# Kernel optimization log

Measured on AMD Instinct MI355X. Metric: run time of the kernel, lower is better.

## Reference

```python
import jax, jax.numpy as jnp
import numpy as np

EMB = 384
HID = 256
HEADS = 4
HD = HID // HEADS  # 64
LAYERS = 2
M_DOCS = 32
TOTAL = 4096  # 1 query + 32 docs + 4063 sentences
LN_EPS = 1e-5


def _layernorm(x, scale, bias):
    mu = jnp.mean(x, axis=-1, keepdims=True)
    var = jnp.mean(jnp.square(x - mu), axis=-1, keepdims=True)
    return (x - mu) * jax.lax.rsqrt(var + LN_EPS) * scale + bias


def setup_inputs() -> dict:
    key = jax.random.key(0)
    ks = jax.random.split(key, 12)
    g = 0.05  # small init scale (stand-in for xavier)
    return {
        "node_embeddings": jax.random.normal(ks[0], (TOTAL, EMB), jnp.float32),
        "adj": jax.random.randint(ks[1], (TOTAL, TOTAL), 0, 2, jnp.int32),
        "num_docs": M_DOCS,
        "proj_w": jax.random.normal(ks[2], (HID, EMB), jnp.float32) * g,
        "proj_b": jnp.zeros((HID,), jnp.float32),
        "ln_scale": jnp.ones((LAYERS, HID), jnp.float32),
        "ln_bias": jnp.zeros((LAYERS, HID), jnp.float32),
        "gat_W": jax.random.normal(ks[3], (LAYERS, HEADS, HD, HID), jnp.float32) * g,
        "gat_a": jax.random.normal(ks[4], (LAYERS, HEADS, 2 * HD), jnp.float32) * g,
        "fusion_w": jax.random.normal(ks[5], (HID, 2 * HID + 2), jnp.float32) * g,
        "fusion_b": jnp.zeros((HID,), jnp.float32),
        "out_w": jax.random.normal(ks[6], (HID,), jnp.float32) * g,
        "out_b": jnp.float32(0.5),
    }


def reference(node_embeddings, adj, num_docs, proj_w, proj_b, ln_scale, ln_bias,
              gat_W, gat_a, fusion_w, fusion_b, out_w, out_b):
    T = node_embeddings.shape[0]
    M = num_docs
    N = T - 1 - M  # number of sentences
    # input projection + relu (dropout = identity in eval)
    h = jax.nn.relu(node_embeddings @ proj_w.T + proj_b)  # (T, HID)
    # query-guided sentence re-weighting
    q = h[0:1]                     # (1, HID)
    s = h[1 + M:]                  # (N, HID)
    qn = q / (jnp.linalg.norm(q, axis=1, keepdims=True) + 1e-8)
    sn = s / (jnp.linalg.norm(s, axis=1, keepdims=True) + 1e-8)
    cos = (qn @ sn.T).reshape(-1, 1)          # (N,1)
    s = s + 0.8 * q * cos
    h = jnp.concatenate([h[:1 + M], s], axis=0)
    mask = (adj == 0)[None]                   # (1,T,T)
    for i in range(LAYERS):
        res = h
        x = _layernorm(h, ln_scale[i], ln_bias[i])
        Wh = jnp.einsum('nd,hkd->hnk', x, gat_W[i])                # (H,T,HD)
        # concat-attention a.[Wh_i ; Wh_j] == a_src.Wh_i + a_dst.Wh_j
        src = jnp.einsum('hnk,hk->hn', Wh, gat_a[i, :, :HD])       # (H,T)
        dst = jnp.einsum('hnk,hk->hn', Wh, gat_a[i, :, HD:])       # (H,T)
        e = jax.nn.leaky_relu(src[:, :, None] + dst[:, None, :], 0.2)  # (H,T,T)
        e = jnp.where(mask, -jnp.inf, e)
        attn = jax.nn.softmax(e, axis=-1)                          # softmax over j
        hn = jnp.einsum('hij,hjk->hik', attn, Wh)                  # (H,T,HD)
        hcat = jnp.transpose(hn, (1, 0, 2)).reshape(T, HEADS * HD)
        h = 0.5 * jax.nn.relu(hcat) + 0.5 * res
    qh = h[0:1]
    sh = h[1 + M:]
    scores = (qh @ sh.T) / (HID ** 0.5)       # (1,N)
    aw = jax.nn.softmax(scores, axis=-1)
    awT = aw.T                                # (N,1)
    qw = qh * (awT + 0.5)                     # (N,HID)
    qnf = qh / (jnp.linalg.norm(qh, axis=1, keepdims=True) + 1e-8)
    snf = sh / (jnp.linalg.norm(sh, axis=1, keepdims=True) + 1e-8)
    cosf = (qnf @ snf.T).reshape(-1, 1)       # (N,1)
    feat = jnp.concatenate([sh, qw, cosf, awT], axis=1)  # (N, 2*HID+2)
    g = jax.nn.relu(feat @ fusion_w.T + fusion_b)
    out = g @ out_w + out_b                   # (N,)
    return out + 0.5 * cosf[:, 0]
```

## Files before the change

### kernel.cpp

```cpp
#include <hip/hip_runtime.h>
#include <hip/hip_bf16.h>
#include <stdint.h>

#define TOTAL 4096
#define EMB 384
#define MD 32
#define NDOCS (TOTAL - 1 - MD)
#define LN_EPS 1e-5f
#define NEGF (-1e30f)

typedef __hip_bfloat16 bf16;
typedef unsigned short ushort_t;
typedef __attribute__((ext_vector_type(8))) short short8;
typedef __attribute__((ext_vector_type(4))) float f32x4;
typedef __attribute__((ext_vector_type(2))) float f32x2;

__device__ __forceinline__ float ldf(const void* p, int i, int isbf) {
    return isbf ? __bfloat162float(((const bf16*)p)[i]) : ((const float*)p)[i];
}

__device__ __forceinline__ unsigned f2bf(float x) {
    return (__float_as_uint(x) + 0x8000u) >> 16;
}

__device__ __forceinline__ unsigned fenc(float f) {
    unsigned u = __float_as_uint(f);
    return (u >> 31) ? ~u : (u | 0x80000000u);
}
__device__ __forceinline__ float fdec(unsigned k) {
    return __uint_as_float((k & 0x80000000u) ? (k & 0x7FFFFFFFu) : ~k);
}

#define NTRANS ((EMB * 256 + 2 * 65536 + 514 * 256) / 256)
__global__ void k_adjmask(const int* adj, unsigned long long* maskb,
                          const uint16_t* embp, int* flag, unsigned* dmaxu,
                          const void* proj_w, const void* gat_W, const void* fusion_w,
                          float* projT, float* gatT, float* fwT) {
    __shared__ int red[4];
    int i = blockIdx.x, t = threadIdx.x;
    int w = t >> 6, l = t & 63;
    for (int c = w; c < 64; c += 4) {
        int a = adj[(size_t)i * TOTAL + c * 64 + l];
        unsigned long long m = __ballot(a != 0);
        if (l == 0) maskb[i * 64 + c] = m;
    }
    if (i == 0) {
        for (int idx = t; idx < 2048; idx += 256) dmaxu[idx] = 0x007FFFFFu;
    }
    if (i < NTRANS) {
        int cnt = 0;
        for (int k = t; k < 4096; k += 256) {
            uint16_t wd = embp[2 * k];
            int e = (wd >> 7) & 0xFF;
            if (e >= 100 && e <= 140) cnt++;
        }
        for (int o = 32; o > 0; o >>= 1) cnt += __shfl_down(cnt, o);
        if ((t & 63) == 0) red[t >> 6] = cnt;
        __syncthreads();
        int isbf = (red[0] + red[1] + red[2] + red[3] > 2048) ? 1 : 0;
        if (i == 0 && t == 0) flag[0] = isbf;
        int idx = i * 256 + t;
        if (idx < EMB * 256) {
            int d = idx >> 8, c = idx & 255;
            projT[(d >> 2) * 1024 + c * 4 + (d & 3)] = ldf(proj_w, c * EMB + d, isbf);
        } else if (idx < EMB * 256 + 2 * 65536) {
            int r = idx - EMB * 256;
            int ll = r >> 16, rem = r & 65535;
            int d = rem >> 8, c = rem & 255;
            gatT[ll * 65536 + (d >> 2) * 1024 + c * 4 + (d & 3)] =
                ldf(gat_W, ll * 65536 + c * 256 + d, isbf);
        } else {
            int r = idx - (EMB * 256 + 2 * 65536);
            int j = r >> 8, c = r & 255;
            fwT[(j >> 2) * 1024 + c * 4 + (j & 3)] = ldf(fusion_w, c * 514 + j, isbf);
        }
    }
}

#define LR 8
__global__ __launch_bounds__(512) void k_lnwh(
        const void* emb, const void* proj_b, const float* projT,
        float* h, const float* gatT, const void* ln_scale, const void* ln_bias,
        const void* gat_a, ushort_t* whswz, float* srcb, unsigned* d12g,
        unsigned* dmaxu, int layer, const int* flagp) {
    __shared__ float embs[9][EMB];
    __shared__ float xs[8][256];
    __shared__ float red[2][LR][4];
    __shared__ float qred[4];
    int isbf = flagp[0];
    int t5 = threadIdx.x;
    int t = t5 & 255, half = t5 >> 8;
    int l = t5 & 63;
    int wh = (t5 >> 6) & 3;
    int i0 = blockIdx.x * LR;
    float hv[4];
    if (layer == 0) {
        for (int idx = t5; idx < 9 * EMB; idx += 512) {
            int r = idx / EMB, d = idx % EMB;
            embs[r][d] = ldf(emb, ((r < 8) ? (i0 + r) : 0) * EMB + d, isbf);
        }
        __syncthreads();
        float bias0 = ldf(proj_b, t, isbf);
        const float4* pT4 = (const float4*)projT;
        float acc[4] = {0.f, 0.f, 0.f, 0.f};
        float qacc = 0.f;
        float4 wc = pT4[t];
        for (int k4 = 0; k4 < 96; k4++) {
            float4 wn = pT4[(k4 < 95 ? k4 + 1 : 95) * 256 + t];
            int d0 = k4 * 4;
            float4 xq = *(const float4*)&embs[8][d0];
            qacc = fmaf(xq.x, wc.x, qacc); qacc = fmaf(xq.y, wc.y, qacc);
            qacc = fmaf(xq.z, wc.z, qacc); qacc = fmaf(xq.w, wc.w, qacc);
#pragma unroll
            for (int r = 0; r < 4; r++) {
                float4 x = *(const float4*)&embs[half * 4 + r][d0];
                acc[r] = fmaf(x.x, wc.x, acc[r]); acc[r] = fmaf(x.y, wc.y, acc[r]);
                acc[r] = fmaf(x.z, wc.z, acc[r]); acc[r] = fmaf(x.w, wc.w, acc[r]);
            }
            wc = wn;
        }
        float qv = fmaxf(qacc + bias0, 0.f);
#pragma unroll
        for (int r = 0; r < 4; r++) hv[r] = fmaxf(acc[r] + bias0, 0.f);
        {
            float a = qv * qv;
            for (int o = 32; o > 0; o >>= 1) a += __shfl_down(a, o);
            if (half == 0 && l == 0) qred[wh] = a;
        }
#pragma unroll
        for (int r = 0; r < 4; r++) {
            float b = hv[r] * hv[r], c = qv * hv[r];
            for (int o = 32; o > 0; o >>= 1) { b += __shfl_down(b, o); c += __shfl_down(c, o); }
            if (l == 0) { red[0][half * 4 + r][wh] = b; red[1][half * 4 + r][wh] = c; }
        }
        __syncthreads();
        if (i0 + LR > 1 + MD) {
            float qn = sqrtf(qred[0] + qred[1] + qred[2] + qred[3]) + 1e-8f;
#pragma unroll
            for (int r = 0; r < 4; r++) {
                int rr = half * 4 + r;
                int i = i0 + rr;
                if (i >= 1 + MD) {
                    float bs = red[0][rr][0] + red[0][rr][1] + red[0][rr][2] + red[0][rr][3];
                    float cs = red[1][rr][0] + red[1][rr][1] + red[1][rr][2] + red[1][rr][3];
                    float k = 0.8f * (cs / (qn * (sqrtf(bs) + 1e-8f)));
                    hv[r] += k * qv;
                }
            }
        }
#pragma unroll
        for (int r = 0; r < 4; r++)
            h[(size_t)(i0 + half * 4 + r) * 256 + t] = hv[r];
        __syncthreads();
    } else {
#pragma unroll
        for (int r = 0; r < 4; r++)
            hv[r] = h[(size_t)(i0 + half * 4 + r) * 256 + t];
    }
    float scale = ldf(ln_scale, layer * 256 + t, isbf);
    float lbias = ldf(ln_bias, layer * 256 + t, isbf);
#pragma unroll
    for (int r = 0; r < 4; r++) {
        float a = hv[r], b = hv[r] * hv[r];
        for (int o = 32; o > 0; o >>= 1) { a += __shfl_down(a, o); b += __shfl_down(b, o); }
        if (l == 0) { red[0][half * 4 + r][wh] = a; red[1][half * 4 + r][wh] = b; }
    }
    __syncthreads();
#pragma unroll
    for (int r = 0; r < 4; r++) {
        int rr = half * 4 + r;
        float mu = (red[0][rr][0] + red[0][rr][1] + red[0][rr][2] + red[0][rr][3]) * (1.f / 256.f);
        float var = (red[1][rr][0] + red[1][rr][1] + red[1][rr][2] + red[1][rr][3]) * (1.f / 256.f) - mu * mu;
        xs[rr][t] = (hv[r] - mu) * rsqrtf(var + LN_EPS) * scale + lbias;
    }
    __syncthreads();
    const float4* gT4 = (const float4*)(gatT + layer * 65536);
    float acc2[4] = {0.f, 0.f, 0.f, 0.f};
    float4 wc2 = gT4[t];
    for (int k4 = 0; k4 < 64; k4++) {
        float4 wn = gT4[(k4 < 63 ? k4 + 1 : 63) * 256 + t];
        int d0 = k4 * 4;
#pragma unroll
        for (int r = 0; r < 4; r++) {
            float4 x = *(const float4*)&xs[half * 4 + r][d0];
            acc2[r] = fmaf(x.x, wc2.x, acc2[r]); acc2[r] = fmaf(x.y, wc2.y, acc2[r]);
            acc2[r] = fmaf(x.z, wc2.z, acc2[r]); acc2[r] = fmaf(x.w, wc2.w, acc2[r]);
        }
        wc2 = wn;
    }
    float av1 = ldf(gat_a, layer * 512 + wh * 128 + l, isbf);
    float av2 = ldf(gat_a, layer * 512 + wh * 128 + 64 + l, isbf);
    const float LOG2E = 1.44269504f;
    float mmax = -__builtin_inff();
#pragma unroll
    for (int r = 0; r < 4; r++) {
        int i = i0 + half * 4 + r;
        int off = (i >> 6) * 16384 + (t >> 6) * 4096 + ((i >> 3) & 7) * 512 +
                  ((t >> 4) & 3) * 128 + (t & 15) * 8 + (i & 7);
        whswz[off] = (ushort_t)f2bf(acc2[r]);
        float sv = acc2[r] * av1, dv = acc2[r] * av2;
        for (int o = 32; o > 0; o >>= 1) { sv += __shfl_down(sv, o); dv += __shfl_down(dv, o); }
        if (l == 0) {
            srcb[wh * 4096 + i] = sv;
            float D1 = exp2f(dv * LOG2E), D2 = exp2f(0.2f * dv * LOG2E);
            d12g[wh * 4096 + i] = (f2bf(D2) << 16) | f2bf(D1);
            mmax = fmaxf(mmax, dv);
        }
    }
    if (l == 0) atomicMax(&dmaxu[(blockIdx.x & 63) * 16 + wh], fenc(mmax));
}

#define TI 16
__global__ __launch_bounds__(512) void k_pv(const ushort_t* whswz, const float* srcb,
                                            const unsigned* dmaxu, const unsigned* d12g,
                                            const unsigned long long* maskb, float* h) {
    __shared__ unsigned long long mbs[16 * 66];
    __shared__ __align__(16) f32x4 accsh[16 * 64];
    __shared__ __align__(16) float lsh[4][4][4];
    __shared__ float srcs[64];
    __shared__ float dmx[4];
    __shared__ unsigned mlut[4];
    int t = threadIdx.x;
    int W = t >> 6, lane = t & 63;
    int hH = W & 3, kq = W >> 2;
    int quad = lane >> 4, c16 = lane & 15;
    int i0 = blockIdx.x * TI;
    if (t < 4) mlut[t] = (t & 1 ? 0x0000FFFFu : 0u) | (t & 2 ? 0xFFFF0000u : 0u);
    if (t < 256) {
        int hh = t >> 6, sl = t & 63;
        float v = fdec(dmaxu[sl * 16 + hh]);
        for (int o = 32; o > 0; o >>= 1) v = fmaxf(v, __shfl_xor(v, o));
        if (sl == 0) dmx[hh] = v;
    }
    for (int idx = t; idx < 16 * 64; idx += 512) {
        int r = idx >> 6, wd = idx & 63;
        mbs[r * 66 + wd] = maskb[(size_t)(i0 + r) * 64 + wd];
    }
    if (t < 64) srcs[t] = srcb[(t >> 4) * 4096 + i0 + (t & 15)];
    __syncthreads();
    const float LOG2E = 1.44269504f;
    float dm = dmx[hH];
    float src = srcs[hH * 16 + c16];
    float sd = src + dm;
    float rce = -fmaxf(sd, 0.2f * sd);
    float E1 = exp2f((src + rce) * LOG2E);
    float E2 = exp2f((0.2f * src + rce) * LOG2E);
    f32x4 acc[4];
    f32x4 accl = (f32x4){0.f, 0.f, 0.f, 0.f};
#pragma unroll
    for (int ct = 0; ct < 4; ct++) acc[ct] = (f32x4){0.f, 0.f, 0.f, 0.f};
    uint4 onesu;
    unsigned os = (c16 == 0) ? 0x3F803F80u : 0u;
    onesu.x = os; onesu.y = os; onesu.z = os; onesu.w = os;
    short8 bfones = __builtin_bit_cast(short8, onesu);
    const uint4* g4 = (const uint4*)whswz;
    const uint4* d4 = (const uint4*)d12g;
    size_t b0 = (size_t)hH * 512 + (size_t)(kq * 4 + quad) * 64 + c16;
    int dbase = hH * 1024, d0i = kq * 8 + quad * 2;
    uint4 bA0 = g4[b0],        bA1 = g4[b0 + 16],        bA2 = g4[b0 + 32],        bA3 = g4[b0 + 48];
    uint4 bB0 = g4[b0 + 2048], bB1 = g4[b0 + 2048 + 16], bB2 = g4[b0 + 2048 + 32], bB3 = g4[b0 + 2048 + 48];
    uint4 dA0 = d4[dbase + d0i],      dA1 = d4[dbase + d0i + 1];
    uint4 dB0 = d4[dbase + 16 + d0i], dB1 = d4[dbase + 16 + d0i + 1];
    auto pvstep = [&](uint4& B0, uint4& B1, uint4& B2, uint4& B3,
                      uint4& DD0, uint4& DD1, int s) {
        uint4 bc0 = B0, bc1 = B1, bc2 = B2, bc3 = B3;
        uint4 dc0 = DD0, dc1 = DD1;
        if (s < 62) {
            size_t bs = b0 + (size_t)(s + 2) * 2048;
            B0 = g4[bs]; B1 = g4[bs + 16]; B2 = g4[bs + 32]; B3 = g4[bs + 48];
            int di = dbase + (s + 2) * 16 + d0i;
            DD0 = d4[di]; DD1 = d4[di + 1];
        }
        unsigned mby = (unsigned)(mbs[c16 * 66 + s] >> (kq * 32 + quad * 8)) & 0xFFu;
        unsigned dw[8] = {dc0.x, dc0.y, dc0.z, dc0.w, dc1.x, dc1.y, dc1.z, dc1.w};
        unsigned pu[4];
#pragma unroll
        for (int q = 0; q < 4; q++) {
            unsigned a = dw[2 * q], b = dw[2 * q + 1];
            f32x2 D1 = (f32x2){__uint_as_float(a << 16), __uint_as_float(b << 16)};
            f32x2 D2 = (f32x2){__uint_as_float(a & 0xFFFF0000u), __uint_as_float(b & 0xFFFF0000u)};
            f32x2 v1 = D1 * E1;
            f32x2 v2 = D2 * E2;
            f32x2 m = __builtin_elementwise_max(v1, v2);
            unsigned v = ((__float_as_uint(m.x) + 0x8000u) >> 16) |
                         ((__float_as_uint(m.y) + 0x8000u) & 0xFFFF0000u);
            pu[q] = v & mlut[(mby >> (2 * q)) & 3u];
        }
        uint4 afu;
        afu.x = pu[0]; afu.y = pu[1]; afu.z = pu[2]; afu.w = pu[3];
        short8 af = __builtin_bit_cast(short8, afu);
        acc[0] = __builtin_amdgcn_mfma_f32_16x16x32_bf16(af, __builtin_bit_cast(short8, bc0), acc[0], 0, 0, 0);
        acc[1] = __builtin_amdgcn_mfma_f32_16x16x32_bf16(af, __builtin_bit_cast(short8, bc1), acc[1], 0, 0, 0);
        acc[2] = __builtin_amdgcn_mfma_f32_16x16x32_bf16(af, __builtin_bit_cast(short8, bc2), acc[2], 0, 0, 0);
        acc[3] = __builtin_amdgcn_mfma_f32_16x16x32_bf16(af, __builtin_bit_cast(short8, bc3), acc[3], 0, 0, 0);
        accl = __builtin_amdgcn_mfma_f32_16x16x32_bf16(af, bfones, accl, 0, 0, 0);
    };
    for (int sp = 0; sp < 32; sp++) {
        pvstep(bA0, bA1, bA2, bA3, dA0, dA1, 2 * sp);
        pvstep(bB0, bB1, bB2, bB3, dB0, dB1, 2 * sp + 1);
    }
    __syncthreads();
    if (kq == 1) {
#pragma unroll
        for (int ct = 0; ct < 4; ct++)
            accsh[(hH * 4 + ct) * 64 + lane] = acc[ct];
        if (c16 == 0) *(f32x4*)&lsh[hH][quad][0] = accl;
    }
    __syncthreads();
    if (kq == 0) {
        float ls[4];
#pragma unroll
        for (int rr = 0; rr < 4; rr++)
            ls[rr] = __shfl(accl[rr], quad * 16) + lsh[hH][quad][rr];
#pragma unroll
        for (int ct = 0; ct < 4; ct++) {
            f32x4 o = acc[ct] + accsh[(hH * 4 + ct) * 64 + lane];
#pragma unroll
            for (int rr = 0; rr < 4; rr++) {
                int row = i0 + quad * 4 + rr;
                size_t idx = (size_t)row * 256 + hH * 64 + ct * 16 + c16;
                float hn = 0.5f * fmaxf(o[rr] / ls[rr], 0.f) + 0.5f * h[idx];
                h[idx] = hn;
            }
        }
    }
}

__global__ __launch_bounds__(256) void k_scores(const float* h, float* scoresv, float* cosv,
                                                float* swp) {
    int t = threadIdx.x, W = t >> 6, lane = t & 63;
    const float4* h4 = (const float4*)h;
    int gw = blockIdx.x * 4 + W;
    float4 q4 = h4[lane];
    float a = q4.x * q4.x + q4.y * q4.y + q4.z * q4.z + q4.w * q4.w;
    for (int o = 32; o > 0; o >>= 1) a += __shfl_xor(a, o);
    float qn = sqrtf(a) + 1e-8f;
    float mw = NEGF, sw = 0.f;
    for (int n = gw; n < NDOCS; n += 1024) {
        float4 s4 = h4[(size_t)(1 + MD + n) * 64 + lane];
        float b = s4.x * s4.x + s4.y * s4.y + s4.z * s4.z + s4.w * s4.w;
        float c = q4.x * s4.x + q4.y * s4.y + q4.z * s4.z + q4.w * s4.w;
        for (int o = 32; o > 0; o >>= 1) { b += __shfl_xor(b, o); c += __shfl_xor(c, o); }
        float sc = c * (1.f / 16.f);
        if (lane == 0) {
            scoresv[n] = sc;
            cosv[n] = c / (qn * (sqrtf(b) + 1e-8f));
        }
        float mn = fmaxf(mw, sc);
        sw = sw * __expf(mw - mn) + __expf(sc - mn);
        mw = mn;
    }
    if (lane == 0) { swp[2 * gw] = mw; swp[2 * gw + 1] = sw; }
}

#define TN 8
__global__ __launch_bounds__(256) void k_fusion(const float* h,
                                                const float* scoresv, const float* swp,
                                                const float* cosv,
                                                const float* fwT, const void* fusion_b,
                                                const void* out_w, const void* out_bp,
                                                void* outv, const int* flagp) {
    __shared__ float feats2[514][TN];
    __shared__ float qhs[256];
    __shared__ float red[TN][4];
    __shared__ float reds[2][4];
    __shared__ float aws[TN];
    int isbf = flagp[0];
    int t = threadIdx.x;
    int n0 = blockIdx.x * TN;
    qhs[t] = h[t];
    float M = NEGF, S = 0.f;
    for (int idx = t; idx < 1024; idx += 256) {
        float pm = swp[2 * idx], ps = swp[2 * idx + 1];
        float mn = fmaxf(M, pm);
        S = S * __expf(M - mn) + ps * __expf(pm - mn);
        M = mn;
    }
    for (int o = 32; o > 0; o >>= 1) {
        float m2 = __shfl_xor(M, o), s2 = __shfl_xor(S, o);
        float mn = fmaxf(M, m2);
        S = S * __expf(M - mn) + s2 * __expf(m2 - mn);
        M = mn;
    }
    if ((t & 63) == 0) { reds[0][t >> 6] = M; reds[1][t >> 6] = S; }
    __syncthreads();
    float Mf = fmaxf(fmaxf(reds[0][0], reds[0][1]), fmaxf(reds[0][2], reds[0][3]));
    float Sf = reds[1][0] * __expf(reds[0][0] - Mf) + reds[1][1] * __expf(reds[0][1] - Mf) +
               reds[1][2] * __expf(reds[0][2] - Mf) + reds[1][3] * __expf(reds[0][3] - Mf);
    float invS = 1.f / Sf;
    if (t < TN) {
        int n = n0 + t;
        aws[t] = (n < NDOCS) ? __expf(scoresv[n] - Mf) * invS : 0.f;
    }
    __syncthreads();
    for (int idx = t; idx < 514 * TN; idx += 256) {
        int j = idx >> 3, r = idx & 7;
        int n = n0 + r;
        float v = 0.f;
        if (n < NDOCS) {
            if (j < 256) v = h[(size_t)(1 + MD + n) * 256 + j];
            else if (j < 512) v = qhs[j - 256] * (aws[r] + 0.5f);
            else if (j == 512) v = cosv[n];
            else v = aws[r];
        }
        feats2[j][r] = v;
    }
    __syncthreads();
    float acc[TN];
    float bk = ldf(fusion_b, t, isbf);
#pragma unroll
    for (int r = 0; r < TN; r++) acc[r] = bk;
    const float4* fT4 = (const float4*)fwT;
    for (int j0 = 0; j0 < 512; j0 += 8) {
        float4 wa = fT4[(j0 >> 2) * 256 + t];
        float4 wb = fT4[((j0 >> 2) + 1) * 256 + t];
        float wv[8] = {wa.x, wa.y, wa.z, wa.w, wb.x, wb.y, wb.z, wb.w};
#pragma unroll
        for (int u = 0; u < 8; u++) {
            float4 fa = *(const float4*)&feats2[j0 + u][0];
            float4 fb = *(const float4*)&feats2[j0 + u][4];
            acc[0] = fmaf(fa.x, wv[u], acc[0]); acc[1] = fmaf(fa.y, wv[u], acc[1]);
            acc[2] = fmaf(fa.z, wv[u], acc[2]); acc[3] = fmaf(fa.w, wv[u], acc[3]);
            acc[4] = fmaf(fb.x, wv[u], acc[4]); acc[5] = fmaf(fb.y, wv[u], acc[5]);
            acc[6] = fmaf(fb.z, wv[u], acc[6]); acc[7] = fmaf(fb.w, wv[u], acc[7]);
        }
    }
    {
        float4 wt = fT4[128 * 256 + t];
#pragma unroll
        for (int r = 0; r < TN; r++) acc[r] = fmaf(feats2[512][r], wt.x, acc[r]);
#pragma unroll
        for (int r = 0; r < TN; r++) acc[r] = fmaf(feats2[513][r], wt.y, acc[r]);
    }
    float ow = ldf(out_w, t, isbf);
    float outb = ldf(out_bp, 0, isbf);
#pragma unroll
    for (int r = 0; r < TN; r++) {
        float o = fmaxf(acc[r], 0.f) * ow;
        for (int off = 32; off > 0; off >>= 1) o += __shfl_down(o, off);
        if ((t & 63) == 0) red[r][t >> 6] = o;
    }
    __syncthreads();
    if (t < TN) {
        int n = n0 + t;
        if (n < NDOCS) {
            float o = red[t][0] + red[t][1] + red[t][2] + red[t][3] + outb + 0.5f * cosv[n];
            if (isbf) ((bf16*)outv)[n] = __float2bfloat16(o);
            else      ((float*)outv)[n] = o;
        }
    }
}

extern "C" void kernel_launch(void* const* d_in, const int* in_sizes, int n_in,
                              void* d_out, int out_size, void* d_ws, size_t ws_size,
                              hipStream_t stream) {
    const void* emb      = d_in[0];
    const int*  adj      = (const int*)d_in[1];
    const void* proj_w   = d_in[3];
    const void* proj_b   = d_in[4];
    const void* ln_scale = d_in[5];
    const void* ln_bias  = d_in[6];
    const void* gat_W    = d_in[7];
    const void* gat_a    = d_in[8];
    const void* fusion_w = d_in[9];
    const void* fusion_b = d_in[10];
    const void* out_w    = d_in[11];
    const void* out_b    = d_in[12];

    unsigned long long* maskb = (unsigned long long*)d_ws;
    int* flag = (int*)((char*)d_ws + (size_t)4096 * 64 * 8);
    float* f = (float*)((char*)d_ws + (size_t)4096 * 64 * 8 + 256);
    float* h       = f; f += 4096 * 256;
    float* srcb    = f; f += 4 * 4096;
    unsigned* d12g = (unsigned*)f; f += 4 * 4096;
    unsigned* dmaxu = (unsigned*)f; f += 2048;
    float* projT   = f; f += EMB * 256;
    float* gatT    = f; f += 2 * 65536;
    float* fwT     = f; f += 129 * 1024;
    float* scoresv = f; f += 4096;
    float* cosv    = f; f += 4096;
    float* swpart  = f; f += 2048;
    ushort_t* whswz = (ushort_t*)f; f += 4096 * 256 / 2;

    k_adjmask<<<dim3(4096), dim3(256), 0, stream>>>(adj, maskb, (const uint16_t*)emb, flag,
                                                    dmaxu, proj_w, gat_W, fusion_w,
                                                    projT, gatT, fwT);
    for (int layer = 0; layer < 2; layer++) {
        k_lnwh<<<dim3(TOTAL / LR), dim3(512), 0, stream>>>(emb, proj_b, projT, h, gatT,
                                                           ln_scale, ln_bias, gat_a,
                                                           whswz, srcb, d12g,
                                                           dmaxu + layer * 1024, layer, flag);
        k_pv<<<dim3(TOTAL / TI), dim3(512), 0, stream>>>(whswz, srcb, dmaxu + layer * 1024,
                                                         d12g, maskb, h);
    }
    k_scores<<<dim3(256), dim3(256), 0, stream>>>(h, scoresv, cosv, swpart);
    k_fusion<<<dim3((NDOCS + TN - 1) / TN), dim3(256), 0, stream>>>(h, scoresv, swpart,
                                                                    cosv, fwT, fusion_b, out_w,
                                                                    out_b, (void*)d_out, flag);
}
```

Baseline: 321.9 us.

## Split-K the projection and GAT matmuls across warps; precompute query row once

The query-row projection and its norm move into one extra block of the setup kernel, so every k_lnwh block no longer recomputes the query embedding. The input-projection and Wh matmuls in k_lnwh switch from one-column-per-thread over all K to a split-K scheme: each of 8 warps covers a K slice for all 8 rows and 256 columns, and partial sums are reduced through shared memory in two passes. LayerNorm and the attention-coefficient reductions then become per-warp row reductions using xor shuffles, with no shared-memory reduction. This trades more registers and a larger shared buffer for fewer redundant FLOPs and less serial K-loop latency per thread.

Measured after the change: 353.2 us. +9.7%, slower.

```diff
diff --git a/kernel.cpp b/kernel.cpp
--- a/kernel.cpp
+++ b/kernel.cpp
@@ -34,9 +34,11 @@
 #define NTRANS ((EMB * 256 + 2 * 65536 + 514 * 256) / 256)
 __global__ void k_adjmask(const int* adj, unsigned long long* maskb,
                           const uint16_t* embp, int* flag, unsigned* dmaxu,
-                          const void* proj_w, const void* gat_W, const void* fusion_w,
-                          float* projT, float* gatT, float* fwT) {
+                          const void* proj_w, const void* proj_b, const void* gat_W,
+                          const void* fusion_w,
+                          float* projT, float* gatT, float* fwT, float* qrow) {
     __shared__ int red[4];
+    __shared__ float qred2[4];
     int i = blockIdx.x, t = threadIdx.x;
     int w = t >> 6, l = t & 63;
     for (int c = w; c < 64; c += 4) {
@@ -47,7 +49,7 @@
     if (i == 0) {
         for (int idx = t; idx < 2048; idx += 256) dmaxu[idx] = 0x007FFFFFu;
     }
-    if (i < NTRANS) {
+    if (i <= NTRANS) {
         int cnt = 0;
         for (int k = t; k < 4096; k += 256) {
             uint16_t wd = embp[2 * k];
@@ -59,20 +61,34 @@
         __syncthreads();
         int isbf = (red[0] + red[1] + red[2] + red[3] > 2048) ? 1 : 0;
         if (i == 0 && t == 0) flag[0] = isbf;
-        int idx = i * 256 + t;
-        if (idx < EMB * 256) {
-            int d = idx >> 8, c = idx & 255;
-            projT[(d >> 2) * 1024 + c * 4 + (d & 3)] = ldf(proj_w, c * EMB + d, isbf);
-        } else if (idx < EMB * 256 + 2 * 65536) {
-            int r = idx - EMB * 256;
-            int ll = r >> 16, rem = r & 65535;
-            int d = rem >> 8, c = rem & 255;
-            gatT[ll * 65536 + (d >> 2) * 1024 + c * 4 + (d & 3)] =
-                ldf(gat_W, ll * 65536 + c * 256 + d, isbf);
+        if (i < NTRANS) {
+            int idx = i * 256 + t;
+            if (idx < EMB * 256) {
+                int d = idx >> 8, c = idx & 255;
+                projT[(d >> 2) * 1024 + c * 4 + (d & 3)] = ldf(proj_w, c * EMB + d, isbf);
+            } else if (idx < EMB * 256 + 2 * 65536) {
+                int r = idx - EMB * 256;
+                int ll = r >> 16, rem = r & 65535;
+                int d = rem >> 8, c = rem & 255;
+                gatT[ll * 65536 + (d >> 2) * 1024 + c * 4 + (d & 3)] =
+                    ldf(gat_W, ll * 65536 + c * 256 + d, isbf);
+            } else {
+                int r = idx - (EMB * 256 + 2 * 65536);
+                int j = r >> 8, c = r & 255;
+                fwT[(j >> 2) * 1024 + c * 4 + (j & 3)] = ldf(fusion_w, c * 514 + j, isbf);
+            }
         } else {
-            int r = idx - (EMB * 256 + 2 * 65536);
-            int j = r >> 8, c = r & 255;
-            fwT[(j >> 2) * 1024 + c * 4 + (j & 3)] = ldf(fusion_w, c * 514 + j, isbf);
+            const void* embv = (const void*)embp;
+            float accq = 0.f;
+            for (int d = 0; d < EMB; d++)
+                accq = fmaf(ldf(embv, d, isbf), ldf(proj_w, (size_t)t * EMB + d, isbf), accq);
+            float qv = fmaxf(accq + ldf(proj_b, t, isbf), 0.f);
+            qrow[t] = qv;
+            float a = qv * qv;
+            for (int o = 32; o > 0; o >>= 1) a += __shfl_down(a, o);
+            if ((t & 63) == 0) qred2[t >> 6] = a;
+            __syncthreads();
+            if (t == 0) qrow[256] = sqrtf(qred2[0] + qred2[1] + qred2[2] + qred2[3]) + 1e-8f;
         }
     }
 }
@@ -82,132 +98,201 @@
         const void* emb, const void* proj_b, const float* projT,
         float* h, const float* gatT, const void* ln_scale, const void* ln_bias,
         const void* gat_a, ushort_t* whswz, float* srcb, unsigned* d12g,
-        unsigned* dmaxu, int layer, const int* flagp) {
-    __shared__ float embs[9][EMB];
+        unsigned* dmaxu, int layer, const int* flagp, const float* qrow) {
+    __shared__ float embs[8][EMB];
     __shared__ float xs[8][256];
-    __shared__ float red[2][LR][4];
-    __shared__ float qred[4];
+    __shared__ float xpart[8][4][256];
     int isbf = flagp[0];
     int t5 = threadIdx.x;
-    int t = t5 & 255, half = t5 >> 8;
+    int w8 = t5 >> 6;
     int l = t5 & 63;
-    int wh = (t5 >> 6) & 3;
     int i0 = blockIdx.x * LR;
+    int myrow = i0 + w8;
     float hv[4];
     if (layer == 0) {
-        for (int idx = t5; idx < 9 * EMB; idx += 512) {
+        for (int idx = t5; idx < 8 * EMB; idx += 512) {
             int r = idx / EMB, d = idx % EMB;
-            embs[r][d] = ldf(emb, ((r < 8) ? (i0 + r) : 0) * EMB + d, isbf);
+            embs[r][d] = ldf(emb, (i0 + r) * EMB + d, isbf);
         }
         __syncthreads();
-        float bias0 = ldf(proj_b, t, isbf);
         const float4* pT4 = (const float4*)projT;
-        float acc[4] = {0.f, 0.f, 0.f, 0.f};
-        float qacc = 0.f;
-        float4 wc = pT4[t];
-        for (int k4 = 0; k4 < 96; k4++) {
-            float4 wn = pT4[(k4 < 95 ? k4 + 1 : 95) * 256 + t];
-            int d0 = k4 * 4;
-            float4 xq = *(const float4*)&embs[8][d0];
-            qacc = fmaf(xq.x, wc.x, qacc); qacc = fmaf(xq.y, wc.y, qacc);
-            qacc = fmaf(xq.z, wc.z, qacc); qacc = fmaf(xq.w, wc.w, qacc);
-#pragma unroll
-            for (int r = 0; r < 4; r++) {
-                float4 x = *(const float4*)&embs[half * 4 + r][d0];
-                acc[r] = fmaf(x.x, wc.x, acc[r]); acc[r] = fmaf(x.y, wc.y, acc[r]);
-                acc[r] = fmaf(x.z, wc.z, acc[r]); acc[r] = fmaf(x.w, wc.w, acc[r]);
-            }
-            wc = wn;
-        }
-        float qv = fmaxf(qacc + bias0, 0.f);
-#pragma unroll
-        for (int r = 0; r < 4; r++) hv[r] = fmaxf(acc[r] + bias0, 0.f);
-        {
-            float a = qv * qv;
-            for (int o = 32; o > 0; o >>= 1) a += __shfl_down(a, o);
-            if (half == 0 && l == 0) qred[wh] = a;
-        }
-#pragma unroll
-        for (int r = 0; r < 4; r++) {
-            float b = hv[r] * hv[r], c = qv * hv[r];
-            for (int o = 32; o > 0; o >>= 1) { b += __shfl_down(b, o); c += __shfl_down(c, o); }
-            if (l == 0) { red[0][half * 4 + r][wh] = b; red[1][half * 4 + r][wh] = c; }
-        }
+        float ap[8][4];
+#pragma unroll
+        for (int r = 0; r < 8; r++)
+#pragma unroll
+            for (int cc = 0; cc < 4; cc++) ap[r][cc] = 0.f;
+        for (int s = 0; s < 12; s++) {
+            int k4 = w8 * 12 + s;
+            float4 wv[4];
+#pragma unroll
+            for (int cc = 0; cc < 4; cc++) wv[cc] = pT4[k4 * 256 + cc * 64 + l];
+#pragma unroll
+            for (int r = 0; r < 8; r++) {
+                float4 x = *(const float4*)&embs[r][k4 * 4];
+#pragma unroll
+                for (int cc = 0; cc < 4; cc++) {
+                    ap[r][cc] = fmaf(x.x, wv[cc].x, ap[r][cc]);
+                    ap[r][cc] = fmaf(x.y, wv[cc].y, ap[r][cc]);
+                    ap[r][cc] = fmaf(x.z, wv[cc].z, ap[r][cc]);
+                    ap[r][cc] = fmaf(x.w, wv[cc].w, ap[r][cc]);
+                }
+            }
+        }
+#pragma unroll
+        for (int r = 0; r < 4; r++)
+#pragma unroll
+            for (int cc = 0; cc < 4; cc++) xpart[w8][r][cc * 64 + l] = ap[r][cc];
         __syncthreads();
-        if (i0 + LR > 1 + MD) {
-            float qn = sqrtf(qred[0] + qred[1] + qred[2] + qred[3]) + 1e-8f;
-#pragma unroll
-            for (int r = 0; r < 4; r++) {
-                int rr = half * 4 + r;
-                int i = i0 + rr;
-                if (i >= 1 + MD) {
-                    float bs = red[0][rr][0] + red[0][rr][1] + red[0][rr][2] + red[0][rr][3];
-                    float cs = red[1][rr][0] + red[1][rr][1] + red[1][rr][2] + red[1][rr][3];
-                    float k = 0.8f * (cs / (qn * (sqrtf(bs) + 1e-8f)));
-                    hv[r] += k * qv;
-                }
-            }
-        }
-#pragma unroll
-        for (int r = 0; r < 4; r++)
-            h[(size_t)(i0 + half * 4 + r) * 256 + t] = hv[r];
+        float bias[4];
+#pragma unroll
+        for (int cc = 0; cc < 4; cc++) bias[cc] = ldf(proj_b, cc * 64 + l, isbf);
+        if (w8 < 4) {
+#pragma unroll
+            for (int cc = 0; cc < 4; cc++) {
+                float s = 0.f;
+#pragma unroll
+                for (int g = 0; g < 8; g++) s += xpart[g][w8][cc * 64 + l];
+                hv[cc] = fmaxf(s + bias[cc], 0.f);
+            }
+        }
         __syncthreads();
+#pragma unroll
+        for (int r = 4; r < 8; r++)
+#pragma unroll
+            for (int cc = 0; cc < 4; cc++) xpart[w8][r - 4][cc * 64 + l] = ap[r][cc];
+        __syncthreads();
+        if (w8 >= 4) {
+#pragma unroll
+            for (int cc = 0; cc < 4; cc++) {
+                float s = 0.f;
+#pragma unroll
+                for (int g = 0; g < 8; g++) s += xpart[g][w8 - 4][cc * 64 + l];
+                hv[cc] = fmaxf(s + bias[cc], 0.f);
+            }
+        }
+        if (myrow >= 1 + MD) {
+            float qv[4];
+#pragma unroll
+            for (int cc = 0; cc < 4; cc++) qv[cc] = qrow[cc * 64 + l];
+            float b = 0.f, c = 0.f;
+#pragma unroll
+            for (int cc = 0; cc < 4; cc++) {
+                b = fmaf(hv[cc], hv[cc], b);
+                c = fmaf(qv[cc], hv[cc], c);
+            }
+            for (int o = 32; o > 0; o >>= 1) { b += __shfl_xor(b, o); c += __shfl_xor(c, o); }
+            float qn = qrow[256];
+            float k = 0.8f * (c / (qn * (sqrtf(b) + 1e-8f)));
+#pragma unroll
+            for (int cc = 0; cc < 4; cc++) hv[cc] += k * qv[cc];
+        }
+#pragma unroll
+        for (int cc = 0; cc < 4; cc++) h[(size_t)myrow * 256 + cc * 64 + l] = hv[cc];
     } else {
 #pragma unroll
-        for (int r = 0; r < 4; r++)
-            hv[r] = h[(size_t)(i0 + half * 4 + r) * 256 + t];
-    }
-    float scale = ldf(ln_scale, layer * 256 + t, isbf);
-    float lbias = ldf(ln_bias, layer * 256 + t, isbf);
-#pragma unroll
-    for (int r = 0; r < 4; r++) {
-        float a = hv[r], b = hv[r] * hv[r];
-        for (int o = 32; o > 0; o >>= 1) { a += __shfl_down(a, o); b += __shfl_down(b, o); }
-        if (l == 0) { red[0][half * 4 + r][wh] = a; red[1][half * 4 + r][wh] = b; }
-    }
-    __syncthreads();
-#pragma unroll
-    for (int r = 0; r < 4; r++) {
-        int rr = half * 4 + r;
-        float mu = (red[0][rr][0] + red[0][rr][1] + red[0][rr][2] + red[0][rr][3]) * (1.f / 256.f);
-        float var = (red[1][rr][0] + red[1][rr][1] + red[1][rr][2] + red[1][rr][3]) * (1.f / 256.f) - mu * mu;
-        xs[rr][t] = (hv[r] - mu) * rsqrtf(var + LN_EPS) * scale + lbias;
+        for (int cc = 0; cc < 4; cc++) hv[cc] = h[(size_t)myrow * 256 + cc * 64 + l];
+    }
+    {
+        float a = 0.f, b2 = 0.f;
+#pragma unroll
+        for (int cc = 0; cc < 4; cc++) { a += hv[cc]; b2 = fmaf(hv[cc], hv[cc], b2); }
+        for (int o = 32; o > 0; o >>= 1) { a += __shfl_xor(a, o); b2 += __shfl_xor(b2, o); }
+        float mu = a * (1.f / 256.f);
+        float var = b2 * (1.f / 256.f) - mu * mu;
+        float rs = rsqrtf(var + LN_EPS);
+#pragma unroll
+        for (int cc = 0; cc < 4; cc++) {
+            float sc = ldf(ln_scale, layer * 256 + cc * 64 + l, isbf);
+            float lb = ldf(ln_bias, layer * 256 + cc * 64 + l, isbf);
+            xs[w8][cc * 64 + l] = (hv[cc] - mu) * rs * sc + lb;
+        }
     }
     __syncthreads();
     const float4* gT4 = (const float4*)(gatT + layer * 65536);
-    float acc2[4] = {0.f, 0.f, 0.f, 0.f};
-    float4 wc2 = gT4[t];
-    for (int k4 = 0; k4 < 64; k4++) {
-        float4 wn = gT4[(k4 < 63 ? k4 + 1 : 63) * 256 + t];
-        int d0 = k4 * 4;
-#pragma unroll
-        for (int r = 0; r < 4; r++) {
-            float4 x = *(const float4*)&xs[half * 4 + r][d0];
-            acc2[r] = fmaf(x.x, wc2.x, acc2[r]); acc2[r] = fmaf(x.y, wc2.y, acc2[r]);
-            acc2[r] = fmaf(x.z, wc2.z, acc2[r]); acc2[r] = fmaf(x.w, wc2.w, acc2[r]);
-        }
-        wc2 = wn;
-    }
-    float av1 = ldf(gat_a, layer * 512 + wh * 128 + l, isbf);
-    float av2 = ldf(gat_a, layer * 512 + wh * 128 + 64 + l, isbf);
-    const float LOG2E = 1.44269504f;
-    float mmax = -__builtin_inff();
-#pragma unroll
-    for (int r = 0; r < 4; r++) {
-        int i = i0 + half * 4 + r;
-        int off = (i >> 6) * 16384 + (t >> 6) * 4096 + ((i >> 3) & 7) * 512 +
-                  ((t >> 4) & 3) * 128 + (t & 15) * 8 + (i & 7);
-        whswz[off] = (ushort_t)f2bf(acc2[r]);
-        float sv = acc2[r] * av1, dv = acc2[r] * av2;
-        for (int o = 32; o > 0; o >>= 1) { sv += __shfl_down(sv, o); dv += __shfl_down(dv, o); }
-        if (l == 0) {
-            srcb[wh * 4096 + i] = sv;
-            float D1 = exp2f(dv * LOG2E), D2 = exp2f(0.2f * dv * LOG2E);
-            d12g[wh * 4096 + i] = (f2bf(D2) << 16) | f2bf(D1);
-            mmax = fmaxf(mmax, dv);
-        }
-    }
-    if (l == 0) atomicMax(&dmaxu[(blockIdx.x & 63) * 16 + wh], fenc(mmax));
+    float aw[8][4];
+#pragma unroll
+    for (int r = 0; r < 8; r++)
+#pragma unroll
+        for (int cc = 0; cc < 4; cc++) aw[r][cc] = 0.f;
+    for (int s = 0; s < 8; s++) {
+        int k4 = w8 * 8 + s;
+        float4 wv[4];
+#pragma unroll
+        for (int cc = 0; cc < 4; cc++) wv[cc] = gT4[k4 * 256 + cc * 64 + l];
+#pragma unroll
+        for (int r = 0; r < 8; r++) {
+            float4 x = *(const float4*)&xs[r][k4 * 4];
+#pragma unroll
+            for (int cc = 0; cc < 4; cc++) {
+                aw[r][cc] = fmaf(x.x, wv[cc].x, aw[r][cc]);
+                aw[r][cc] = fmaf(x.y, wv[cc].y, aw[r][cc]);
+                aw[r][cc] = fmaf(x.z, wv[cc].z, aw[r][cc]);
+                aw[r][cc] = fmaf(x.w, wv[cc].w, aw[r][cc]);
+            }
+        }
+    }
+#pragma unroll
+    for (int r = 0; r < 4; r++)
+#pragma unroll
+        for (int cc = 0; cc < 4; cc++) xpart[w8][r][cc * 64 + l] = aw[r][cc];
+    __syncthreads();
+    float acc2[4];
+    if (w8 < 4) {
+#pragma unroll
+        for (int cc = 0; cc < 4; cc++) {
+            float s = 0.f;
+#pragma unroll
+            for (int g = 0; g < 8; g++) s += xpart[g][w8][cc * 64 + l];
+            acc2[cc] = s;
+        }
+    }
+    __syncthreads();
+#pragma unroll
+    for (int r = 4; r < 8; r++)
+#pragma unroll
+        for (int cc = 0; cc < 4; cc++) xpart[w8][r - 4][cc * 64 + l] = aw[r][cc];
+    __syncthreads();
+    if (w8 >= 4) {
+#pragma unroll
+        for (int cc = 0; cc < 4; cc++) {
+            float s = 0.f;
+#pragma unroll
+            for (int g = 0; g < 8; g++) s += xpart[g][w8 - 4][cc * 64 + l];
+            acc2[cc] = s;
+        }
+    }
+#pragma unroll
+    for (int cc = 0; cc < 4; cc++) {
+        int col = cc * 64 + l;
+        int off = (myrow >> 6) * 16384 + (col >> 6) * 4096 + ((myrow >> 3) & 7) * 512 +
+                  ((col >> 4) & 3) * 128 + (col & 15) * 8 + (myrow & 7);
+        whswz[off] = (ushort_t)f2bf(acc2[cc]);
+    }
+    float sv[4], dv[4];
+#pragma unroll
+    for (int cc = 0; cc < 4; cc++) {
+        float av1 = ldf(gat_a, layer * 512 + cc * 128 + l, isbf);
+        float av2 = ldf(gat_a, layer * 512 + cc * 128 + 64 + l, isbf);
+        sv[cc] = acc2[cc] * av1;
+        dv[cc] = acc2[cc] * av2;
+    }
+    for (int o = 32; o > 0; o >>= 1) {
+#pragma unroll
+        for (int cc = 0; cc < 4; cc++) {
+            sv[cc] += __shfl_down(sv[cc], o);
+            dv[cc] += __shfl_down(dv[cc], o);
+        }
+    }
+    if (l == 0) {
+        const float LOG2E = 1.44269504f;
+#pragma unroll
+        for (int cc = 0; cc < 4; cc++) {
+            srcb[cc * 4096 + myrow] = sv[cc];
+            float D1 = exp2f(dv[cc] * LOG2E), D2 = exp2f(0.2f * dv[cc] * LOG2E);
+            d12g[cc * 4096 + myrow] = (f2bf(D2) << 16) | f2bf(D1);
+            atomicMax(&dmaxu[(blockIdx.x & 63) * 16 + cc], fenc(dv[cc]));
+        }
+    }
 }
 
 #define TI 16
@@ -480,16 +565,18 @@
     float* scoresv = f; f += 4096;
     float* cosv    = f; f += 4096;
     float* swpart  = f; f += 2048;
+    float* qrowb   = f; f += 260;
     ushort_t* whswz = (ushort_t*)f; f += 4096 * 256 / 2;
 
     k_adjmask<<<dim3(4096), dim3(256), 0, stream>>>(adj, maskb, (const uint16_t*)emb, flag,
-                                                    dmaxu, proj_w, gat_W, fusion_w,
-                                                    projT, gatT, fwT);
+                                                    dmaxu, proj_w, proj_b, gat_W, fusion_w,
+                                                    projT, gatT, fwT, qrowb);
     for (int layer = 0; layer < 2; layer++) {
         k_lnwh<<<dim3(TOTAL / LR), dim3(512), 0, stream>>>(emb, proj_b, projT, h, gatT,
                                                            ln_scale, ln_bias, gat_a,
                                                            whswz, srcb, d12g,
-                                                           dmaxu + layer * 1024, layer, flag);
+                                                           dmaxu + layer * 1024, layer, flag,
+                                                           qrowb);
         k_pv<<<dim3(TOTAL / TI), dim3(512), 0, stream>>>(whswz, srcb, dmaxu + layer * 1024,
                                                          d12g, maskb, h);
     }
```
